# Performance work log

Measured on AMD Instinct MI355X. Metric: run time of the kernel, lower is better.

Reference implementation:

```python
import jax, jax.numpy as jnp
import numpy as np
import math

NUM_BANDS = 8
BINS = 512
CROPSIZE = 1024
BATCH = 4


def _dwconv(x, w, b):
    # depthwise Conv1d, kernel=3, padding=1, groups=C. x: [B,C,W], w: [C,1,3], b: [C]
    y = jax.lax.conv_general_dilated(x, w, window_strides=(1,), padding=((1, 1),),
                                     feature_group_count=x.shape[1])
    return y + b[None, :, None]


def setup_inputs() -> dict:
    key = jax.random.key(0)
    ks = jax.random.split(key, 20)
    s = 0.02
    lin = lambda k: jax.random.normal(k, (BINS, BINS), jnp.float32) * s
    cw = lambda k: jax.random.normal(k, (BINS, 1, 3), jnp.float32) * s
    vec = lambda k: jax.random.normal(k, (BINS,), jnp.float32) * s
    return {
        "x": jax.random.normal(ks[0], (BATCH, CROPSIZE, BINS), jnp.float32),
        "q_w": lin(ks[1]), "q_b": vec(ks[2]), "q_cw": cw(ks[3]), "q_cb": vec(ks[4]),
        "k_w": lin(ks[5]), "k_b": vec(ks[6]), "k_cw": cw(ks[7]), "k_cb": vec(ks[8]),
        "v_w": lin(ks[9]), "v_b": vec(ks[10]), "v_cw": cw(ks[11]), "v_cb": vec(ks[12]),
        "o_w": lin(ks[13]), "o_b": vec(ks[14]),
        "er": jax.random.normal(ks[15], (BINS // NUM_BANDS, CROPSIZE), jnp.float32),
    }


def reference(x, q_w, q_b, q_cw, q_cb, k_w, k_b, k_cw, k_cb,
              v_w, v_b, v_cw, v_cb, o_w, o_b, er):
    b, w, c = x.shape
    h = NUM_BANDS

    def proj(lw, lb, cwt, cbt):
        y = x @ lw.T + lb                                   # [b,w,c] linear
        y = _dwconv(y.transpose(0, 2, 1), cwt, cbt)         # [b,c,w] depthwise conv
        return y.transpose(0, 2, 1).reshape(b, w, h, -1)    # [b,w,h,d]

    q = proj(q_w, q_b, q_cw, q_cb).transpose(0, 2, 1, 3)    # [b,h,w,d]
    k = proj(k_w, k_b, k_cw, k_cb).transpose(0, 2, 3, 1)    # [b,h,d,w]
    v = proj(v_w, v_b, v_cw, v_cb).transpose(0, 2, 1, 3)    # [b,h,w,d]

    # relative position bias via pad/transpose/slice skew
    qe = jnp.einsum('bhwd,dc->bhwc', q, er)                 # [b,h,w,cropsize]
    p = jnp.pad(qe, ((0, 0), (0, 0), (0, 0), (1, 0)))       # [b,h,w,cs+1]
    p = p.transpose(0, 1, 3, 2)[:, :, 1:, :]                # [b,h,cs,w] == [b,h,w,w]

    qk = (q @ k + p) / math.sqrt(c)
    a = jax.nn.softmax(qk, axis=-1)
    out = (a @ v).transpose(0, 2, 1, 3).reshape(b, w, c)    # [b,w,c]
    return out @ o_w.T + o_b
```

## Files before the change

kernel.cpp:

```cpp
#include <hip/hip_runtime.h>
#include <hip/hip_bf16.h>
#include <math.h>


#define CROP 1024
#define NB 512
#define NH 8
#define HD 64
#define NBATCH 4
#define MTOT 4096
#define NBH 32
#define JSPLIT 2
#define ROWS_TOT 32768

typedef __attribute__((ext_vector_type(8))) short bf8;
typedef __attribute__((ext_vector_type(4))) short s4;
typedef __attribute__((ext_vector_type(4))) float f4;
typedef __attribute__((ext_vector_type(8))) _Float16 h8;

__device__ __forceinline__ short f2bf(float f) {
  __hip_bfloat16 h = __float2bfloat16(f);
  short s;
  __builtin_memcpy(&s, &h, 2);
  return s;
}
__device__ __forceinline__ float bf2f(short s) {
  union { unsigned u; float f; } v; v.u = ((unsigned)(unsigned short)s) << 16;
  return v.f;
}
__device__ __forceinline__ f4 mfma16(bf8 a, bf8 b, f4 c) {
  return __builtin_amdgcn_mfma_f32_16x16x32_bf16(a, b, c, 0, 0, 0);
}
__device__ __forceinline__ float fast_exp2(float x) {
#if __has_builtin(__builtin_amdgcn_exp2f)
  return __builtin_amdgcn_exp2f(x);
#else
  float r;
  asm("v_exp_f32 %0, %1" : "=v"(r) : "v"(x));
  return r;
#endif
}

__device__ __forceinline__ void stage16(const short* g, short* ldsbase, int lane) {
#if __has_builtin(__builtin_amdgcn_global_load_lds)
  __builtin_amdgcn_global_load_lds(
      (const __attribute__((address_space(1))) void*)g,
      (__attribute__((address_space(3))) void*)ldsbase, 16, 0, 0);
#else
  *(bf8*)(ldsbase + lane * 8) = *(const bf8*)g;
#endif
}

#define ISC 0.044194173824159216f
#define QSCALE 0.06376743237228177f

__global__ __launch_bounds__(256) void prep_kernel(
    const float* __restrict__ x,
    const float* __restrict__ w0, const float* __restrict__ w1,
    const float* __restrict__ w2, const float* __restrict__ w3,
    const float* __restrict__ er,
    short* __restrict__ xb, short* __restrict__ wb, short* __restrict__ erT)
{
  const int blk = blockIdx.x;
  const int t = threadIdx.x;
  if (blk < 1024) {
    int i = (blk * 256 + t) * 8;
    f4 a = *(const f4*)(x + i);
    f4 b = *(const f4*)(x + i + 4);
    bf8 o;
#pragma unroll
    for (int j = 0; j < 4; ++j) { o[j] = f2bf(a[j]); o[4 + j] = f2bf(b[j]); }
    *(bf8*)(xb + i) = o;
  } else if (blk < 1536) {
    int p = (blk - 1024) >> 7;
    const float* s = (p == 0) ? w0 : (p == 1) ? w1 : (p == 2) ? w2 : w3;
    int i = (((blk - 1024) & 127) * 256 + t) * 8;
    f4 a = *(const f4*)(s + i);
    f4 b = *(const f4*)(s + i + 4);
    bf8 o;
#pragma unroll
    for (int j = 0; j < 4; ++j) { o[j] = f2bf(a[j]); o[4 + j] = f2bf(b[j]); }
    *(bf8*)(wb + (size_t)p * NB * NB + i) = o;
  } else {
    int idx = (blk - 1536) * 256 + t;
    int w = idx >> 6, d = idx & 63;
    erT[idx] = f2bf(er[d * CROP + w]);
  }
}

__device__ __forceinline__ void gemm128_loop(
    const short* __restrict__ A, const short* __restrict__ Bm,
    short* As, short* Bs, int rowA0, int rowB0, f4 (&acc)[4][4], int t)
{
  const int lane = t & 63, wave = t >> 6;
  const int wr = wave >> 1, wc = wave & 1;
  const int l15 = lane & 15, l4 = lane >> 4;
  const int crow = lane >> 3;
  const int csub = lane & 7;
  const int kb = (csub * 16) ^ (crow << 4);

  for (int k0 = 0; k0 < NB; k0 += 64) {
    __syncthreads();
#pragma unroll
    for (int i = 0; i < 4; ++i) {
      const int c = wave * 4 + i;
      stage16(A + (size_t)(rowA0 + c * 8 + crow) * NB + k0 + (kb >> 1),
              As + c * 512, lane);
      stage16(Bm + (size_t)(rowB0 + c * 8 + crow) * NB + k0 + (kb >> 1),
              Bs + c * 512, lane);
    }
    __syncthreads();
#pragma unroll
    for (int ks = 0; ks < 2; ++ks) {
      bf8 af[4], bg[4];
#pragma unroll
      for (int mt = 0; mt < 4; ++mt) {
        const int row = wr * 64 + mt * 16 + l15;
        const int byt = (ks * 64 + l4 * 16) ^ ((row & 7) << 4);
        af[mt] = *(const bf8*)&As[row * 64 + (byt >> 1)];
      }
#pragma unroll
      for (int nt = 0; nt < 4; ++nt) {
        const int row = wc * 64 + nt * 16 + l15;
        const int byt = (ks * 64 + l4 * 16) ^ ((row & 7) << 4);
        bg[nt] = *(const bf8*)&Bs[row * 64 + (byt >> 1)];
      }
#pragma unroll
      for (int mt = 0; mt < 4; ++mt)
#pragma unroll
        for (int nt = 0; nt < 4; ++nt)
          acc[mt][nt] = mfma16(af[mt], bg[nt], acc[mt][nt]);
    }
  }
}

__global__ __launch_bounds__(256) void proj_gemm3(
    const short* __restrict__ Xb, const short* __restrict__ Wb,
    const float* __restrict__ B0, const float* __restrict__ B1, const float* __restrict__ B2,
    short* __restrict__ O0, short* __restrict__ O1, short* __restrict__ O2)
{
  __shared__ short As[128 * 64];
  __shared__ short Bs[128 * 64];
  f4 acc[4][4];
#pragma unroll
  for (int i = 0; i < 4; ++i)
#pragma unroll
    for (int j = 0; j < 4; ++j) acc[i][j] = (f4){0.f, 0.f, 0.f, 0.f};

  const int bm = blockIdx.x, bn = blockIdx.y;
  gemm128_loop(Xb, Wb, As, Bs, bm * 128, bn * 128, acc, threadIdx.x);

  const int p = bn >> 2;
  const float* Bb = (p == 0) ? B0 : (p == 1) ? B1 : B2;
  short* Out = (p == 0) ? O0 : (p == 1) ? O1 : O2;
  const int ncol0 = (bn & 3) * 128;

  const int t = threadIdx.x;
  const int lane = t & 63, wave = t >> 6;
  const int wr = wave >> 1, wc = wave & 1;
  const int l15 = lane & 15, l4 = lane >> 4;
#pragma unroll
  for (int mt = 0; mt < 4; ++mt)
#pragma unroll
    for (int nt = 0; nt < 4; ++nt) {
      const int col = ncol0 + wc * 64 + nt * 16 + l15;
      const float bias = Bb[col];
#pragma unroll
      for (int r = 0; r < 4; ++r) {
        const int row = bm * 128 + wr * 64 + mt * 16 + l4 * 4 + r;
        Out[(size_t)row * NB + col] = f2bf(acc[mt][nt][r] + bias);
      }
    }
}

__global__ __launch_bounds__(256) void dwconv_all(
    const short* __restrict__ q0p, const short* __restrict__ k0p,
    const short* __restrict__ v0p,
    const float* __restrict__ qcw, const float* __restrict__ qcb,
    const float* __restrict__ kcw, const float* __restrict__ kcb,
    const float* __restrict__ vcw, const float* __restrict__ vcb,
    short* __restrict__ qb, short* __restrict__ kb, short* __restrict__ vb)
{
  const int blk = blockIdx.x;
  const int t = threadIdx.x;

  if (blk < 2048) {
    const int p = blk >> 10;
    const short* src = p ? k0p : q0p;
    const float* cw = p ? kcw : qcw;
    const float* cb = p ? kcb : qcb;
    short* dst = p ? kb : qb;
    const float scale = p ? 1.0f : QSCALE;

    const int idx = ((blk & 1023) * 256 + t) * 8;
    const int c = idx & (NB - 1);
    const int m = idx >> 9;
    const int w = m & (CROP - 1);
    const int b = m >> 10;

    const bf8 z = (bf8){0, 0, 0, 0, 0, 0, 0, 0};
    bf8 mid = *(const bf8*)(src + idx);
    bf8 lo = (w > 0) ? *(const bf8*)(src + idx - NB) : z;
    bf8 hi = (w < CROP - 1) ? *(const bf8*)(src + idx + NB) : z;

    f4 cwv[6];
#pragma unroll
    for (int i = 0; i < 6; ++i) cwv[i] = *(const f4*)(cw + c * 3 + i * 4);
    f4 cb0 = *(const f4*)(cb + c);
    f4 cb1 = *(const f4*)(cb + c + 4);

    bf8 o;
#pragma unroll
    for (int j = 0; j < 8; ++j) {
      float k0w = cwv[(3 * j) >> 2][(3 * j) & 3];
      float k1w = cwv[(3 * j + 1) >> 2][(3 * j + 1) & 3];
      float k2w = cwv[(3 * j + 2) >> 2][(3 * j + 2) & 3];
      float bias = (j < 4) ? cb0[j] : cb1[j - 4];
      float acc = bias + k0w * bf2f(lo[j]) + k1w * bf2f(mid[j]) + k2w * bf2f(hi[j]);
      o[j] = f2bf(acc * scale);
    }
    const int h = c >> 6, d0 = c & 63;
    *(bf8*)(dst + ((size_t)(b * NH + h) * CROP + w) * HD + d0) = o;
  } else {
    __shared__ short S[66][72];
    const int blk2 = blk - 2048;
    const int w0 = (blk2 & 15) * 64, c0 = ((blk2 >> 4) & 7) * 64, b = blk2 >> 7;

#pragma unroll
    for (int i = 0; i < 3; ++i) {
      int r = i * 32 + (t >> 3);
      if (r < 66) {
        int w = w0 - 1 + r;
        int cg = (t & 7) * 8;
        bf8 val = (bf8){0, 0, 0, 0, 0, 0, 0, 0};
        if (w >= 0 && w < CROP)
          val = *(const bf8*)(v0p + ((size_t)b * CROP + w) * NB + c0 + cg);
        *(bf8*)&S[r][cg] = val;
      }
    }
    __syncthreads();

    const int c = t & 63, wv = t >> 6;
    const float k0w = vcw[(c0 + c) * 3 + 0];
    const float k1w = vcw[(c0 + c) * 3 + 1];
    const float k2w = vcw[(c0 + c) * 3 + 2];
    const float bias = vcb[c0 + c];

    float xa = bf2f(S[wv * 16][c]);
    float xb2 = bf2f(S[wv * 16 + 1][c]);
    short res[16];
#pragma unroll
    for (int ww = 0; ww < 16; ++ww) {
      float xc = bf2f(S[wv * 16 + ww + 2][c]);
      res[ww] = f2bf(bias + k0w * xa + k1w * xb2 + k2w * xc);
      xa = xb2; xb2 = xc;
    }
    short* dstbase = vb + ((size_t)(b * NB) + c0 + c) * CROP + w0
                     + (wv >> 1) * 32 + (wv & 1) * 4;
#pragma unroll
    for (int pidx = 0; pidx < 4; ++pidx)
      *(s4*)(dstbase + pidx * 8) = *(s4*)&res[pidx * 4];
  }
}

__global__ __launch_bounds__(512) void attn_part(
    const short* __restrict__ Qb, const short* __restrict__ Kb,
    const short* __restrict__ Vb, const short* __restrict__ ErT,
    _Float16* __restrict__ Op, float* __restrict__ lbuf)
{
  __shared__ short Ks[64][72];
  __shared__ short Qs[64][72];
  __shared__ short Vs[64][72];

  const int L = blockIdx.x;
  const int xcd = L & 7;
  const int slot = L >> 3;
  const int grp = xcd * 8 + (slot >> 3);
  const int qt = slot & 7;
  const int bh = grp >> 1;
  const int s = grp & 1;

  const int t = threadIdx.x;
  const int lane = t & 63, wave = t >> 6;
  const int l15 = lane & 15, l4 = lane >> 4;
  const int wq = qt * 128 + wave * 16;

  bf8 qa[2], ea[2];
  {
    const short* qrow = Qb + ((size_t)bh * CROP + wq + l15) * HD + l4 * 8;
    qa[0] = *(const bf8*)(qrow);
    qa[1] = *(const bf8*)(qrow + 32);
    const short* erow = ErT + (size_t)(wq + l15) * HD + l4 * 8;
    ea[0] = *(const bf8*)(erow);
    ea[1] = *(const bf8*)(erow + 32);
  }

  const short ONEBF = 0x3F80;
  const bf8 vones = (bf8){ONEBF, ONEBF, ONEBF, ONEBF, ONEBF, ONEBF, ONEBF, ONEBF};

  f4 lsacc = (f4){0.f, 0.f, 0.f, 0.f};
  f4 oacc[4];
#pragma unroll
  for (int nt = 0; nt < 4; ++nt) oacc[nt] = (f4){0.f, 0.f, 0.f, 0.f};

  const int sr2 = t >> 3, sc2 = (t & 7) * 8;
  const short* ksrc = Kb + ((size_t)bh * CROP + sr2) * HD + sc2;
  const short* qsrc = Qb + ((size_t)bh * CROP + sr2) * HD + sc2;
  const short* vsrc = Vb + ((size_t)bh * HD + sr2) * CROP + sc2;

  const int jbase = s * (CROP / JSPLIT);
  const int JLEN = CROP / JSPLIT;

  bf8 rk = *(const bf8*)(ksrc + jbase * HD);
  bf8 rq = *(const bf8*)(qsrc + jbase * HD);
  bf8 rv = *(const bf8*)(vsrc + jbase);

  for (int jj = 0; jj < JLEN; jj += 64) {
    __syncthreads();
    *(bf8*)&Ks[sr2][sc2] = rk;
    *(bf8*)&Qs[sr2][sc2] = rq;
    *(bf8*)&Vs[sr2][sc2] = rv;
    __syncthreads();

    const int jn = jj + 64;
    if (jn < JLEN) {
      rk = *(const bf8*)(ksrc + (jbase + jn) * HD);
      rq = *(const bf8*)(qsrc + (jbase + jn) * HD);
      rv = *(const bf8*)(vsrc + jbase + jn);
    }

    f4 sacc[4];
#pragma unroll
    for (int nt = 0; nt < 4; ++nt) sacc[nt] = (f4){0.f, 0.f, 0.f, 0.f};
    __builtin_amdgcn_s_setprio(1);
#pragma unroll
    for (int ks = 0; ks < 2; ++ks) {
#pragma unroll
      for (int nt = 0; nt < 4; ++nt) {
        bf8 kf = *(bf8*)&Ks[nt * 16 + l15][ks * 32 + l4 * 8];
        sacc[nt] = mfma16(kf, qa[ks], sacc[nt]);
        bf8 qf = *(bf8*)&Qs[nt * 16 + l15][ks * 32 + l4 * 8];
        sacc[nt] = mfma16(qf, ea[ks], sacc[nt]);
      }
    }
    __builtin_amdgcn_s_setprio(0);

    bf8 pf0, pf1;
#pragma unroll
    for (int nt = 0; nt < 4; ++nt) {
      float e0 = fast_exp2(sacc[nt][0]);
      float e1 = fast_exp2(sacc[nt][1]);
      float e2 = fast_exp2(sacc[nt][2]);
      float e3 = fast_exp2(sacc[nt][3]);
      if (nt < 2) {
        pf0[nt * 4 + 0] = f2bf(e0); pf0[nt * 4 + 1] = f2bf(e1);
        pf0[nt * 4 + 2] = f2bf(e2); pf0[nt * 4 + 3] = f2bf(e3);
      } else {
        pf1[(nt - 2) * 4 + 0] = f2bf(e0); pf1[(nt - 2) * 4 + 1] = f2bf(e1);
        pf1[(nt - 2) * 4 + 2] = f2bf(e2); pf1[(nt - 2) * 4 + 3] = f2bf(e3);
      }
    }

    __builtin_amdgcn_s_setprio(1);
#pragma unroll
    for (int ks = 0; ks < 2; ++ks) {
      bf8 pf = ks ? pf1 : pf0;
#pragma unroll
      for (int nt = 0; nt < 4; ++nt) {
        bf8 vf = *(bf8*)&Vs[nt * 16 + l15][ks * 32 + l4 * 8];
        oacc[nt] = mfma16(pf, vf, oacc[nt]);
      }
      lsacc = mfma16(pf, vones, lsacc);
    }
    __builtin_amdgcn_s_setprio(0);
  }

#pragma unroll
  for (int r = 0; r < 4; ++r) {
    const int row = wq + l4 * 4 + r;
    const size_t ridx = (size_t)(s * NBH + bh) * CROP + row;
#pragma unroll
    for (int nt = 0; nt < 4; ++nt)
      Op[ridx * HD + nt * 16 + l15] = (_Float16)oacc[nt][r];
  }
  if (l15 == 0) {
#pragma unroll
    for (int r = 0; r < 4; ++r)
      lbuf[(size_t)(s * NBH + bh) * CROP + wq + l4 * 4 + r] = lsacc[r];
  }
}

__global__ __launch_bounds__(256) void attn_combine(
    const _Float16* __restrict__ Op, const float* __restrict__ lbuf,
    short* __restrict__ Ao)
{
  const int t = threadIdx.x;
  const int idx = blockIdx.x * 32 + (t >> 3);
  const int dth = (t & 7) * 8;
  float l = 0.f;
#pragma unroll
  for (int s = 0; s < JSPLIT; ++s) l += lbuf[(size_t)s * ROWS_TOT + idx];
  float inv = 1.f / l;
  float o[8] = {0, 0, 0, 0, 0, 0, 0, 0};
#pragma unroll
  for (int s = 0; s < JSPLIT; ++s) {
    h8 v = *(const h8*)(Op + ((size_t)s * ROWS_TOT + idx) * HD + dth);
#pragma unroll
    for (int j = 0; j < 8; ++j) o[j] += (float)v[j];
  }
  const int bh = idx >> 10, row = idx & (CROP - 1);
  const int b = bh >> 3, h = bh & 7;
  short* dst = Ao + ((size_t)(b * CROP + row)) * NB + h * HD + dth;
  bf8 ov;
#pragma unroll
  for (int j = 0; j < 8; ++j) ov[j] = f2bf(o[j] * inv);
  *(bf8*)dst = ov;
}

__global__ __launch_bounds__(256) void out_gemm2(
    const short* __restrict__ A, const short* __restrict__ Wt,
    const float* __restrict__ Bb, float* __restrict__ Out)
{
  __shared__ short As[64][72];
  __shared__ short Bs[64][72];
  const int t = threadIdx.x;
  const int lane = t & 63, wave = t >> 6;
  const int wr = wave >> 1, wc = wave & 1;
  const int l15 = lane & 15, l4 = lane >> 4;
  const int bm = blockIdx.x, bn = blockIdx.y;

  f4 acc[2][2];
#pragma unroll
  for (int i = 0; i < 2; ++i)
#pragma unroll
    for (int j = 0; j < 2; ++j) acc[i][j] = (f4){0.f, 0.f, 0.f, 0.f};

  const int sr = t >> 2, sc = (t & 3) * 16;
  const short* arow = A + (size_t)(bm * 64 + sr) * NB + sc;
  const short* wrow = Wt + (size_t)(bn * 64 + sr) * NB + sc;

  for (int k0 = 0; k0 < NB; k0 += 64) {
    bf8 a0 = *(const bf8*)(arow + k0);
    bf8 a1 = *(const bf8*)(arow + k0 + 8);
    bf8 b0 = *(const bf8*)(wrow + k0);
    bf8 b1 = *(const bf8*)(wrow + k0 + 8);
    __syncthreads();
    *(bf8*)&As[sr][sc] = a0;
    *(bf8*)&As[sr][sc + 8] = a1;
    *(bf8*)&Bs[sr][sc] = b0;
    *(bf8*)&Bs[sr][sc + 8] = b1;
    __syncthreads();
#pragma unroll
    for (int ks = 0; ks < 2; ++ks) {
      bf8 af[2], bg[2];
#pragma unroll
      for (int mt = 0; mt < 2; ++mt)
        af[mt] = *(bf8*)&As[wr * 32 + mt * 16 + l15][ks * 32 + l4 * 8];
#pragma unroll
      for (int nt = 0; nt < 2; ++nt)
        bg[nt] = *(bf8*)&Bs[wc * 32 + nt * 16 + l15][ks * 32 + l4 * 8];
#pragma unroll
      for (int mt = 0; mt < 2; ++mt)
#pragma unroll
        for (int nt = 0; nt < 2; ++nt)
          acc[mt][nt] = mfma16(af[mt], bg[nt], acc[mt][nt]);
    }
  }
#pragma unroll
  for (int mt = 0; mt < 2; ++mt)
#pragma unroll
    for (int nt = 0; nt < 2; ++nt)
#pragma unroll
      for (int r = 0; r < 4; ++r) {
        int row = bm * 64 + wr * 32 + mt * 16 + l4 * 4 + r;
        int col = bn * 64 + wc * 32 + nt * 16 + l15;
        Out[(size_t)row * NB + col] = acc[mt][nt][r] + Bb[col];
      }
}

extern "C" void kernel_launch(void* const* d_in, const int* in_sizes, int n_in,
                              void* d_out, int out_size, void* d_ws, size_t ws_size,
                              hipStream_t stream) {
  (void)in_sizes; (void)n_in; (void)out_size; (void)ws_size;
  const float* x    = (const float*)d_in[0];
  const float* q_w  = (const float*)d_in[1];
  const float* q_b  = (const float*)d_in[2];
  const float* q_cw = (const float*)d_in[3];
  const float* q_cb = (const float*)d_in[4];
  const float* k_w  = (const float*)d_in[5];
  const float* k_b  = (const float*)d_in[6];
  const float* k_cw = (const float*)d_in[7];
  const float* k_cb = (const float*)d_in[8];
  const float* v_w  = (const float*)d_in[9];
  const float* v_b  = (const float*)d_in[10];
  const float* v_cw = (const float*)d_in[11];
  const float* v_cb = (const float*)d_in[12];
  const float* o_w  = (const float*)d_in[13];
  const float* o_b  = (const float*)d_in[14];
  const float* er   = (const float*)d_in[15];
  float* out = (float*)d_out;

  char* ws = (char*)d_ws;
  const size_t MB = 1u << 20;
  short* q0  = (short*)(ws + 0 * MB);
  short* k0  = (short*)(ws + 4 * MB);
  short* v0  = (short*)(ws + 8 * MB);
  short* qb2 = (short*)(ws + 12 * MB);
  short* kb2 = (short*)(ws + 16 * MB);
  short* vb2 = (short*)(ws + 20 * MB);
  short* ao  = (short*)(ws + 24 * MB);
  short* erT = (short*)(ws + 28 * MB);
  short* xb  = (short*)(ws + 29 * MB);
  short* wb  = (short*)(ws + 33 * MB);
  _Float16* Op = (_Float16*)(ws + 36 * MB);
  float* lbuf  = (float*)(ws + 52 * MB);

  prep_kernel<<<dim3(1792), dim3(256), 0, stream>>>(
      x, q_w, k_w, v_w, o_w, er, xb, wb, erT);
  proj_gemm3<<<dim3(32, 12), dim3(256), 0, stream>>>(
      xb, wb, q_b, k_b, v_b, q0, k0, v0);
  dwconv_all<<<dim3(2560), dim3(256), 0, stream>>>(
      q0, k0, v0, q_cw, q_cb, k_cw, k_cb, v_cw, v_cb, qb2, kb2, vb2);
  attn_part<<<dim3(512), dim3(512), 0, stream>>>(
      qb2, kb2, vb2, erT, Op, lbuf);
  attn_combine<<<dim3(1024), dim3(256), 0, stream>>>(Op, lbuf, ao);
  out_gemm2<<<dim3(64, 8), dim3(256), 0, stream>>>(
      ao, wb + 3 * NB * NB, o_b, out);
}
```

Baseline: 62.80 us.

## Remove key-split in attention and normalize output in-kernel, dropping combine pass

The attention kernel no longer splits the key dimension into two halves. Each block now processes all 1024 keys for its query tile and writes normalized bf16 output directly. This removes the fp16 partial-output and row-sum buffers and the separate combine kernel launch, saving global traffic and one launch. In exchange the grid halves to 256 blocks of 512 threads, which may underfill the 256-CU device and doubles the serial loop length per block.

```diff
diff --git a/kernel.cpp b/kernel.cpp
--- a/kernel.cpp
+++ b/kernel.cpp
@@ -10,13 +10,10 @@
 #define NBATCH 4
 #define MTOT 4096
 #define NBH 32
-#define JSPLIT 2
-#define ROWS_TOT 32768
 
 typedef __attribute__((ext_vector_type(8))) short bf8;
 typedef __attribute__((ext_vector_type(4))) short s4;
 typedef __attribute__((ext_vector_type(4))) float f4;
-typedef __attribute__((ext_vector_type(8))) _Float16 h8;
 
 __device__ __forceinline__ short f2bf(float f) {
   __hip_bfloat16 h = __float2bfloat16(f);
@@ -263,10 +260,10 @@
   }
 }
 
-__global__ __launch_bounds__(512) void attn_part(
+__global__ __launch_bounds__(512) void attn_full(
     const short* __restrict__ Qb, const short* __restrict__ Kb,
     const short* __restrict__ Vb, const short* __restrict__ ErT,
-    _Float16* __restrict__ Op, float* __restrict__ lbuf)
+    short* __restrict__ Ao)
 {
   __shared__ short Ks[64][72];
   __shared__ short Qs[64][72];
@@ -275,10 +272,8 @@
   const int L = blockIdx.x;
   const int xcd = L & 7;
   const int slot = L >> 3;
-  const int grp = xcd * 8 + (slot >> 3);
+  const int bh = xcd * 4 + (slot >> 3);
   const int qt = slot & 7;
-  const int bh = grp >> 1;
-  const int s = grp & 1;
 
   const int t = threadIdx.x;
   const int lane = t & 63, wave = t >> 6;
@@ -308,14 +303,11 @@
   const short* qsrc = Qb + ((size_t)bh * CROP + sr2) * HD + sc2;
   const short* vsrc = Vb + ((size_t)bh * HD + sr2) * CROP + sc2;
 
-  const int jbase = s * (CROP / JSPLIT);
-  const int JLEN = CROP / JSPLIT;
-
-  bf8 rk = *(const bf8*)(ksrc + jbase * HD);
-  bf8 rq = *(const bf8*)(qsrc + jbase * HD);
-  bf8 rv = *(const bf8*)(vsrc + jbase);
-
-  for (int jj = 0; jj < JLEN; jj += 64) {
+  bf8 rk = *(const bf8*)(ksrc);
+  bf8 rq = *(const bf8*)(qsrc);
+  bf8 rv = *(const bf8*)(vsrc);
+
+  for (int jj = 0; jj < CROP; jj += 64) {
     __syncthreads();
     *(bf8*)&Ks[sr2][sc2] = rk;
     *(bf8*)&Qs[sr2][sc2] = rq;
@@ -323,10 +315,10 @@
     __syncthreads();
 
     const int jn = jj + 64;
-    if (jn < JLEN) {
-      rk = *(const bf8*)(ksrc + (jbase + jn) * HD);
-      rq = *(const bf8*)(qsrc + (jbase + jn) * HD);
-      rv = *(const bf8*)(vsrc + jbase + jn);
+    if (jn < CROP) {
+      rk = *(const bf8*)(ksrc + jn * HD);
+      rq = *(const bf8*)(qsrc + jn * HD);
+      rv = *(const bf8*)(vsrc + jn);
     }
 
     f4 sacc[4];
@@ -375,46 +367,16 @@
     __builtin_amdgcn_s_setprio(0);
   }
 
+  const int b = bh >> 3, h = bh & 7;
 #pragma unroll
   for (int r = 0; r < 4; ++r) {
+    const float inv = 1.f / lsacc[r];
     const int row = wq + l4 * 4 + r;
-    const size_t ridx = (size_t)(s * NBH + bh) * CROP + row;
+    short* dst = Ao + ((size_t)(b * CROP + row)) * NB + h * HD;
 #pragma unroll
     for (int nt = 0; nt < 4; ++nt)
-      Op[ridx * HD + nt * 16 + l15] = (_Float16)oacc[nt][r];
-  }
-  if (l15 == 0) {
-#pragma unroll
-    for (int r = 0; r < 4; ++r)
-      lbuf[(size_t)(s * NBH + bh) * CROP + wq + l4 * 4 + r] = lsacc[r];
-  }
-}
-
-__global__ __launch_bounds__(256) void attn_combine(
-    const _Float16* __restrict__ Op, const float* __restrict__ lbuf,
-    short* __restrict__ Ao)
-{
-  const int t = threadIdx.x;
-  const int idx = blockIdx.x * 32 + (t >> 3);
-  const int dth = (t & 7) * 8;
-  float l = 0.f;
-#pragma unroll
-  for (int s = 0; s < JSPLIT; ++s) l += lbuf[(size_t)s * ROWS_TOT + idx];
-  float inv = 1.f / l;
-  float o[8] = {0, 0, 0, 0, 0, 0, 0, 0};
-#pragma unroll
-  for (int s = 0; s < JSPLIT; ++s) {
-    h8 v = *(const h8*)(Op + ((size_t)s * ROWS_TOT + idx) * HD + dth);
-#pragma unroll
-    for (int j = 0; j < 8; ++j) o[j] += (float)v[j];
-  }
-  const int bh = idx >> 10, row = idx & (CROP - 1);
-  const int b = bh >> 3, h = bh & 7;
-  short* dst = Ao + ((size_t)(b * CROP + row)) * NB + h * HD + dth;
-  bf8 ov;
-#pragma unroll
-  for (int j = 0; j < 8; ++j) ov[j] = f2bf(o[j] * inv);
-  *(bf8*)dst = ov;
+      dst[nt * 16 + l15] = f2bf(oacc[nt][r] * inv);
+  }
 }
 
 __global__ __launch_bounds__(256) void out_gemm2(
@@ -512,8 +474,6 @@
   short* erT = (short*)(ws + 28 * MB);
   short* xb  = (short*)(ws + 29 * MB);
   short* wb  = (short*)(ws + 33 * MB);
-  _Float16* Op = (_Float16*)(ws + 36 * MB);
-  float* lbuf  = (float*)(ws + 52 * MB);
 
   prep_kernel<<<dim3(1792), dim3(256), 0, stream>>>(
       x, q_w, k_w, v_w, o_w, er, xb, wb, erT);
@@ -521,9 +481,8 @@
       xb, wb, q_b, k_b, v_b, q0, k0, v0);
   dwconv_all<<<dim3(2560), dim3(256), 0, stream>>>(
       q0, k0, v0, q_cw, q_cb, k_cw, k_cb, v_cw, v_cb, qb2, kb2, vb2);
-  attn_part<<<dim3(512), dim3(512), 0, stream>>>(
-      qb2, kb2, vb2, erT, Op, lbuf);
-  attn_combine<<<dim3(1024), dim3(256), 0, stream>>>(Op, lbuf, ao);
+  attn_full<<<dim3(256), dim3(512), 0, stream>>>(
+      qb2, kb2, vb2, erT, ao);
   out_gemm2<<<dim3(64, 8), dim3(256), 0, stream>>>(
       ao, wb + 3 * NB * NB, o_b, out);
 }
```

New measurement: 62.73 us (median of 2 runs). About the same (-0.1%).
